# Kernel tuning notes

Hardware: AMD Instinct MI355X
Metric: run time of the kernel (lower is better)

The kernel has to match this reference:

```python
import jax, jax.numpy as jnp
import numpy as np

SAMPLE_RATE = 44100.0
MIN_GAIN, MAX_GAIN = -12.0, 12.0
MIN_Q, MAX_Q = 0.1, 10.0
# (min, max) for the 15 normalized control params, in channel order
PARAM_RANGES = np.array([
    (MIN_GAIN, MAX_GAIN), (20.0, 2000.0), (MIN_Q, MAX_Q),      # low shelf
    (MIN_GAIN, MAX_GAIN), (20.0, 200.0), (MIN_Q, MAX_Q),       # band0 peaking
    (MIN_GAIN, MAX_GAIN), (200.0, 2000.0), (MIN_Q, MAX_Q),     # band1 peaking
    (MIN_GAIN, MAX_GAIN), (2000.0, 12000.0), (MIN_Q, MAX_Q),   # band2 peaking
    (MIN_GAIN, MAX_GAIN), (4000.0, 16000.0), (MIN_Q, MAX_Q),   # high shelf
], dtype=np.float32)


def _biquad(gain_db, f0, q, ftype):
    """RBJ cookbook biquad. Inputs shape (bs,), returns (bs, 6) normalized so a0==1."""
    A = 10.0 ** (gain_db / 40.0)
    w0 = 2.0 * jnp.pi * (f0 / SAMPLE_RATE)
    alpha = jnp.sin(w0) / (2.0 * q)
    cw = jnp.cos(w0)
    sA = jnp.sqrt(A)
    if ftype == 'peaking':
        b0 = 1.0 + alpha * A; b1 = -2.0 * cw; b2 = 1.0 - alpha * A
        a0 = 1.0 + alpha / A; a1 = -2.0 * cw; a2 = 1.0 - alpha / A
    elif ftype == 'low_shelf':
        b0 = A * ((A + 1) - (A - 1) * cw + 2 * sA * alpha)
        b1 = 2 * A * ((A - 1) - (A + 1) * cw)
        b2 = A * ((A + 1) - (A - 1) * cw - 2 * sA * alpha)
        a0 = (A + 1) + (A - 1) * cw + 2 * sA * alpha
        a1 = -2 * ((A - 1) + (A + 1) * cw)
        a2 = (A + 1) + (A - 1) * cw - 2 * sA * alpha
    else:  # high_shelf
        b0 = A * ((A + 1) + (A - 1) * cw + 2 * sA * alpha)
        b1 = -2 * A * ((A - 1) + (A + 1) * cw)
        b2 = A * ((A + 1) + (A - 1) * cw - 2 * sA * alpha)
        a0 = (A + 1) - (A - 1) * cw + 2 * sA * alpha
        a1 = 2 * ((A - 1) - (A + 1) * cw)
        a2 = (A + 1) - (A - 1) * cw - 2 * sA * alpha
    coeffs = jnp.stack([b0, b1, b2, a0, a1, a2], axis=-1)
    return coeffs / a0[..., None]


def _compute_sos(p):
    """p: (bs, 15) denormalized params -> sos (bs, 5, 6)."""
    secs = [
        _biquad(p[:, 0], p[:, 1], p[:, 2], 'low_shelf'),
        _biquad(p[:, 3], p[:, 4], p[:, 5], 'peaking'),
        _biquad(p[:, 6], p[:, 7], p[:, 8], 'peaking'),
        _biquad(p[:, 9], p[:, 10], p[:, 11], 'peaking'),
        _biquad(p[:, 12], p[:, 13], p[:, 14], 'high_shelf'),
    ]
    return jnp.stack(secs, axis=1)


def _sosfilt(sos, x):
    """Cascaded 5-section biquad, direct form II transposed, zero initial state.
    sos: (bs, 5, 6), x: (bs, T) -> (bs, T)."""
    b0, b1, b2 = sos[..., 0], sos[..., 1], sos[..., 2]  # each (bs, 5)
    a1, a2 = sos[..., 4], sos[..., 5]

    def step(carry, xt):
        z1, z2 = carry  # (bs, 5) each
        s = xt  # (bs,)
        z1n, z2n = [], []
        for k in range(5):  # fixed small cascade
            y = b0[:, k] * s + z1[:, k]
            z1n.append(b1[:, k] * s - a1[:, k] * y + z2[:, k])
            z2n.append(b2[:, k] * s - a2[:, k] * y)
            s = y
        return (jnp.stack(z1n, 1), jnp.stack(z2n, 1)), s

    bs = x.shape[0]
    z0 = jnp.zeros((bs, 5), x.dtype)
    _, y = jax.lax.scan(step, (z0, z0), x.T)
    return y.T


def setup_inputs() -> dict:
    key = jax.random.key(0)
    k1, k2 = jax.random.split(key)
    x = jax.random.normal(k1, (32, 1, 131072), dtype=jnp.float32)
    control_params = jax.random.uniform(k2, (32, 15, 1), dtype=jnp.float32)
    return {"x": x, "control_params": control_params}


def reference(x, control_params):
    # denormalize: min + p * (max - min)
    lo = jnp.asarray(PARAM_RANGES[:, 0])
    hi = jnp.asarray(PARAM_RANGES[:, 1])
    p = control_params[:, :, 0]  # (bs, 15)
    p_denorm = lo[None, :] + p * (hi - lo)[None, :]
    sos = _compute_sos(p_denorm)           # (bs, 5, 6)
    y = _sosfilt(sos, x[:, 0, :])          # (bs, T)
    return y[:, None, :], sos
```

## Files before the change

kernel.cpp:

```cpp
#include <hip/hip_runtime.h>
#include <math.h>


#define NB 32
#define LCH 16
#define T_LEN 131072
#define CPB 256
#define BPB 32
#define WPB 128
#define NPOW 13
#define PROW 12
#define PMAT (10 * PROW)

__constant__ double c_lo[15] = {-12.0,   20.0, 0.1,
                                -12.0,   20.0, 0.1,
                                -12.0,  200.0, 0.1,
                                -12.0, 2000.0, 0.1,
                                -12.0, 4000.0, 0.1};
__constant__ double c_hi[15] = { 12.0,  2000.0, 10.0,
                                 12.0,   200.0, 10.0,
                                 12.0,  2000.0, 10.0,
                                 12.0, 12000.0, 10.0,
                                 12.0, 16000.0, 10.0};

__global__ __launch_bounds__(128)
void eq_setup(const float* __restrict__ cp, float* __restrict__ sos_out,
              float* __restrict__ powers)
{
    int b = blockIdx.x;
    int t = threadIdx.x;
    __shared__ float  sc[5][5];
    __shared__ double Abuf[2][10][10];

    if (t < 5) {
        int k = t;
        double p[3];
#pragma unroll
        for (int j = 0; j < 3; ++j) {
            int i = k * 3 + j;
            double pv = (double)cp[b * 15 + i];
            p[j] = c_lo[i] + pv * (c_hi[i] - c_lo[i]);
        }
        double A     = exp(p[0] * (M_LN10 / 40.0));
        double w0    = 2.0 * M_PI * p[1] / 44100.0;
        double alpha = sin(w0) / (2.0 * p[2]);
        double cw    = cos(w0);
        double sA    = sqrt(A);
        double b0, b1, b2, a0, a1, a2;
        if (k == 0) {
            b0 =     A * ((A + 1) - (A - 1) * cw + 2 * sA * alpha);
            b1 = 2 * A * ((A - 1) - (A + 1) * cw);
            b2 =     A * ((A + 1) - (A - 1) * cw - 2 * sA * alpha);
            a0 =          (A + 1) + (A - 1) * cw + 2 * sA * alpha;
            a1 =    -2 * ((A - 1) + (A + 1) * cw);
            a2 =          (A + 1) + (A - 1) * cw - 2 * sA * alpha;
        } else if (k == 4) {
            b0 =     A * ((A + 1) + (A - 1) * cw + 2 * sA * alpha);
            b1 = -2 * A * ((A - 1) + (A + 1) * cw);
            b2 =     A * ((A + 1) + (A - 1) * cw - 2 * sA * alpha);
            a0 =          (A + 1) - (A - 1) * cw + 2 * sA * alpha;
            a1 =     2 * ((A - 1) - (A + 1) * cw);
            a2 =          (A + 1) - (A - 1) * cw - 2 * sA * alpha;
        } else {
            b0 = 1.0 + alpha * A;
            b1 = -2.0 * cw;
            b2 = 1.0 - alpha * A;
            a0 = 1.0 + alpha / A;
            a1 = -2.0 * cw;
            a2 = 1.0 - alpha / A;
        }
        double inv = 1.0 / a0;
        float fb0 = (float)(b0 * inv), fb1 = (float)(b1 * inv), fb2 = (float)(b2 * inv);
        float fa1 = (float)(a1 * inv), fa2 = (float)(a2 * inv);
        float* o = sos_out + (size_t)(b * 5 + k) * 6;
        o[0] = fb0; o[1] = fb1; o[2] = fb2; o[3] = 1.0f; o[4] = fa1; o[5] = fa2;
        sc[k][0] = fb0; sc[k][1] = fb1; sc[k][2] = fb2; sc[k][3] = fa1; sc[k][4] = fa2;
    }
    __syncthreads();

    if (t < 10) {
        double z[10];
#pragma unroll
        for (int i = 0; i < 10; ++i) z[i] = 0.0;
        z[t] = 1.0;
        double s = 0.0;
        double zn[10];
#pragma unroll
        for (int k = 0; k < 5; ++k) {
            double b0 = sc[k][0], b1 = sc[k][1], b2 = sc[k][2];
            double a1 = sc[k][3], a2 = sc[k][4];
            double y = b0 * s + z[2 * k];
            zn[2 * k]     = b1 * s - a1 * y + z[2 * k + 1];
            zn[2 * k + 1] = b2 * s - a2 * y;
            s = y;
        }
#pragma unroll
        for (int r = 0; r < 10; ++r) Abuf[0][r][t] = zn[r];
    }
    __syncthreads();

    int r = t / 10, cc = t % 10;
    int cur = 0;
    for (int sq = 0; sq < 16; ++sq) {
        double acc = 0.0;
        if (t < 100) {
#pragma unroll
            for (int j = 0; j < 10; ++j) acc += Abuf[cur][r][j] * Abuf[cur][j][cc];
        }
        __syncthreads();
        if (t < 100) Abuf[cur ^ 1][r][cc] = acc;
        __syncthreads();
        cur ^= 1;
        if (sq >= 3 && t < 100) {
            int m = sq - 3;
            powers[((size_t)b * NPOW + m) * 100 + t] = (float)Abuf[cur][r][cc];
        }
    }
}

template<bool ACC>
__device__ __forceinline__ void affineT(const float* __restrict__ P,
                                        const float u[10], float v[10])
{
#pragma unroll
    for (int rr = 0; rr < 10; ++rr) {
        const float* rp = P + rr * PROW;
        float a = ACC ? v[rr] : 0.0f;
#pragma unroll
        for (int c = 0; c <= (rr | 1); ++c) a = fmaf(rp[c], u[c], a);
        v[rr] = a;
    }
}

__device__ __forceinline__ void matvecT(const float* __restrict__ P, float v[10])
{
    float u[10];
#pragma unroll
    for (int i = 0; i < 10; ++i) u[i] = v[i];
    affineT<false>(P, u, v);
}

__device__ __forceinline__ void stagePl(float* Pl, const float* __restrict__ powers,
                                        int b, int tid, int nthr)
{
    const float* src = powers + (size_t)b * NPOW * 100;
    for (int i = tid; i < NPOW * PMAT; i += nthr) {
        int c = i % PROW;
        int r = (i / PROW) % 10;
        int m = i / PMAT;
        Pl[i] = (c < 10) ? src[m * 100 + r * 10 + c] : 0.0f;
    }
}

__global__ __launch_bounds__(256)
void eq_pass1(const float* __restrict__ x, const float* __restrict__ sos,
              const float* __restrict__ powers, float* __restrict__ wt)
{
    int blk = blockIdx.x;
    int b = blk >> 5, sp = blk & (BPB - 1);
    int tid = threadIdx.x;
    int w = tid >> 6, lw = tid & 63;

    __shared__ float Pl[NPOW * PMAT];
    stagePl(Pl, powers, b, tid, 256);

    const float* s5 = sos + (size_t)(b * 5) * 6;
    float cb0[5], cb1[5], cb2[5], ca1[5], ca2[5];
#pragma unroll
    for (int k = 0; k < 5; ++k) {
        cb0[k] = s5[k * 6 + 0]; cb1[k] = s5[k * 6 + 1]; cb2[k] = s5[k * 6 + 2];
        ca1[k] = s5[k * 6 + 4]; ca2[k] = s5[k * 6 + 5];
    }

    int c = sp * CPB + tid;
    const float* xp = x + (size_t)b * T_LEN + (size_t)c * LCH;
    float xr[LCH];
#pragma unroll
    for (int t0 = 0; t0 < LCH; t0 += 4) {
        float4 xv = *reinterpret_cast<const float4*>(xp + t0);
        xr[t0] = xv.x; xr[t0 + 1] = xv.y; xr[t0 + 2] = xv.z; xr[t0 + 3] = xv.w;
    }

    float z1[5] = {0, 0, 0, 0, 0}, z2[5] = {0, 0, 0, 0, 0};
#pragma unroll
    for (int j = 0; j < LCH; ++j) {
        float s = xr[j];
#pragma unroll
        for (int k = 0; k < 5; ++k) {
            float yk = fmaf(cb0[k], s, z1[k]);
            float u  = fmaf(cb1[k], s, z2[k]);
            z1[k] = fmaf(-ca1[k], yk, u);
            z2[k] = fmaf(-ca2[k], yk, cb2[k] * s);
            s = yk;
        }
    }
    float sv[10];
#pragma unroll
    for (int k = 0; k < 5; ++k) { sv[2 * k] = z1[k]; sv[2 * k + 1] = z2[k]; }

    __syncthreads();

#pragma unroll
    for (int j = 0; j < 6; ++j) {
        const float* P = Pl + j * PMAT;
        float u[10];
#pragma unroll
        for (int i = 0; i < 10; ++i) u[i] = __shfl_up(sv[i], 1 << j);
        if (lw >= (1 << j)) affineT<true>(P, u, sv);
    }

    if (lw == 63) {
        int wid = sp * 4 + w;
        float* wp = wt + (size_t)(b * WPB + wid) * 10;
#pragma unroll
        for (int i = 0; i < 10; ++i) wp[i] = sv[i];
    }
}

__global__ __launch_bounds__(64)
void eq_scan(const float* __restrict__ powers, const float* __restrict__ wt,
             float* __restrict__ seeds)
{
    int b = blockIdx.x;
    int l = threadIdx.x;

    __shared__ float Pl[NPOW * PMAT];
    stagePl(Pl, powers, b, l, 64);
    __syncthreads();

    const float* wp = wt + (size_t)(b * WPB + 2 * l) * 10;
    float t0[10], t1[10];
#pragma unroll
    for (int i = 0; i < 10; ++i) { t0[i] = wp[i]; t1[i] = wp[10 + i]; }

    float tau[10];
#pragma unroll
    for (int i = 0; i < 10; ++i) tau[i] = t1[i];
    affineT<true>(Pl + 6 * PMAT, t0, tau);

#pragma unroll
    for (int j = 0; j < 6; ++j) {
        const float* P = Pl + (7 + j) * PMAT;
        float u[10];
#pragma unroll
        for (int i = 0; i < 10; ++i) u[i] = __shfl_up(tau[i], 1 << j);
        if (l >= (1 << j)) affineT<true>(P, u, tau);
    }

    float e[10];
#pragma unroll
    for (int i = 0; i < 10; ++i) e[i] = __shfl_up(tau[i], 1);
    if (l == 0) {
#pragma unroll
        for (int i = 0; i < 10; ++i) e[i] = 0.0f;
    }

    float s1[10];
#pragma unroll
    for (int i = 0; i < 10; ++i) s1[i] = t0[i];
    affineT<true>(Pl + 6 * PMAT, e, s1);

    float* sp0 = seeds + (size_t)(b * WPB + 2 * l) * 10;
#pragma unroll
    for (int i = 0; i < 10; ++i) { sp0[i] = e[i]; sp0[10 + i] = s1[i]; }
}

__global__ __launch_bounds__(256)
void eq_pass2(const float* __restrict__ x, const float* __restrict__ sos,
              const float* __restrict__ powers, const float* __restrict__ seeds,
              float* __restrict__ y)
{
    int blk = blockIdx.x;
    int b = blk >> 5, sp = blk & (BPB - 1);
    int tid = threadIdx.x;
    int w = tid >> 6, lw = tid & 63;

    __shared__ float Pl[NPOW * PMAT];
    __shared__ float ys[CPB * 17];
    stagePl(Pl, powers, b, tid, 256);

    const float* s5 = sos + (size_t)(b * 5) * 6;
    float cb0[5], cb1[5], cb2[5], ca1[5], ca2[5];
#pragma unroll
    for (int k = 0; k < 5; ++k) {
        cb0[k] = s5[k * 6 + 0]; cb1[k] = s5[k * 6 + 1]; cb2[k] = s5[k * 6 + 2];
        ca1[k] = s5[k * 6 + 4]; ca2[k] = s5[k * 6 + 5];
    }

    int c = sp * CPB + tid;
    const float* xp = x + (size_t)b * T_LEN + (size_t)c * LCH;
    float xr[LCH];
#pragma unroll
    for (int t0 = 0; t0 < LCH; t0 += 4) {
        float4 xv = *reinterpret_cast<const float4*>(xp + t0);
        xr[t0] = xv.x; xr[t0 + 1] = xv.y; xr[t0 + 2] = xv.z; xr[t0 + 3] = xv.w;
    }

    float z1[5] = {0, 0, 0, 0, 0}, z2[5] = {0, 0, 0, 0, 0};
#pragma unroll
    for (int j = 0; j < LCH; ++j) {
        float s = xr[j];
#pragma unroll
        for (int k = 0; k < 5; ++k) {
            float yk = fmaf(cb0[k], s, z1[k]);
            float u  = fmaf(cb1[k], s, z2[k]);
            z1[k] = fmaf(-ca1[k], yk, u);
            z2[k] = fmaf(-ca2[k], yk, cb2[k] * s);
            s = yk;
        }
    }
    float sv[10];
#pragma unroll
    for (int k = 0; k < 5; ++k) { sv[2 * k] = z1[k]; sv[2 * k + 1] = z2[k]; }

    __syncthreads();

#pragma unroll
    for (int j = 0; j < 6; ++j) {
        const float* P = Pl + j * PMAT;
        float u[10];
#pragma unroll
        for (int i = 0; i < 10; ++i) u[i] = __shfl_up(sv[i], 1 << j);
        if (lw >= (1 << j)) affineT<true>(P, u, sv);
    }
    float es[10];
#pragma unroll
    for (int i = 0; i < 10; ++i) es[i] = __shfl_up(sv[i], 1);
    if (lw == 0) {
#pragma unroll
        for (int i = 0; i < 10; ++i) es[i] = 0.0f;
    }

    int wid = sp * 4 + w;
    const float* sdp = seeds + (size_t)(b * WPB + wid) * 10;
    float F[10];
#pragma unroll
    for (int i = 0; i < 10; ++i) F[i] = sdp[i];
#pragma unroll
    for (int m = 0; m < 6; ++m) {
        if ((lw >> m) & 1) matvecT(Pl + m * PMAT, F);
    }
#pragma unroll
    for (int k = 0; k < 5; ++k) {
        z1[k] = F[2 * k]     + es[2 * k];
        z2[k] = F[2 * k + 1] + es[2 * k + 1];
    }

    float* yl = ys + tid * 17;
#pragma unroll
    for (int j = 0; j < LCH; ++j) {
        float s = xr[j];
#pragma unroll
        for (int k = 0; k < 5; ++k) {
            float yk = fmaf(cb0[k], s, z1[k]);
            float u  = fmaf(cb1[k], s, z2[k]);
            z1[k] = fmaf(-ca1[k], yk, u);
            z2[k] = fmaf(-ca2[k], yk, cb2[k] * s);
            s = yk;
        }
        yl[j] = s;
    }
    __syncthreads();

    float* yg = y + (size_t)b * T_LEN + (size_t)sp * (CPB * LCH);
#pragma unroll
    for (int it = 0; it < (CPB * LCH) / (256 * 4); ++it) {
        int i = (tid + it * 256) * 4;
        int p = (i >> 4) * 17 + (i & 15);
        *reinterpret_cast<float4*>(yg + i) =
            make_float4(ys[p], ys[p + 1], ys[p + 2], ys[p + 3]);
    }
}

extern "C" void kernel_launch(void* const* d_in, const int* in_sizes, int n_in,
                              void* d_out, int out_size, void* d_ws, size_t ws_size,
                              hipStream_t stream)
{
    const float* x  = (const float*)d_in[0];
    const float* cp = (const float*)d_in[1];
    float* out = (float*)d_out;
    float* sos = out + (size_t)NB * T_LEN;

    float* powers = (float*)d_ws;
    float* wt     = powers + (size_t)NB * NPOW * 100;
    float* seeds  = wt + (size_t)NB * WPB * 10;

    eq_setup<<<dim3(NB), dim3(128), 0, stream>>>(cp, sos, powers);
    eq_pass1<<<dim3(NB * BPB), dim3(256), 0, stream>>>(x, sos, powers, wt);
    eq_scan <<<dim3(NB), dim3(64), 0, stream>>>(powers, wt, seeds);
    eq_pass2<<<dim3(NB * BPB), dim3(256), 0, stream>>>(x, sos, powers, seeds, out);
}
```

Baseline: 50.63 us.

## Store per-chunk exclusive scan states in pass1 so pass2 skips recomputation

Pass1 now computes each thread's exclusive in-warp state prefix and writes it to a global workspace, so pass2 no longer reruns the zero-state filter pass and the warp scan; it reads that prefix and filters once. The shared-memory staging of the power matrices is dropped, and matrices are read directly from global memory, which removes a sync and the LDS footprint. Launch bounds now request 4 blocks per CU. This trades recomputation for extra global traffic (10 floats per thread written and read back) and relies on cache hits for the matrix reads.

```diff
diff --git a/kernel.cpp b/kernel.cpp
--- a/kernel.cpp
+++ b/kernel.cpp
@@ -7,10 +7,9 @@
 #define T_LEN 131072
 #define CPB 256
 #define BPB 32
+#define CCH 8192
 #define WPB 128
 #define NPOW 13
-#define PROW 12
-#define PMAT (10 * PROW)
 
 __constant__ double c_lo[15] = {-12.0,   20.0, 0.1,
                                 -12.0,   20.0, 0.1,
@@ -124,7 +123,7 @@
 {
 #pragma unroll
     for (int rr = 0; rr < 10; ++rr) {
-        const float* rp = P + rr * PROW;
+        const float* rp = P + rr * 10;
         float a = ACC ? v[rr] : 0.0f;
 #pragma unroll
         for (int c = 0; c <= (rr | 1); ++c) a = fmaf(rp[c], u[c], a);
@@ -140,29 +139,15 @@
     affineT<false>(P, u, v);
 }
 
-__device__ __forceinline__ void stagePl(float* Pl, const float* __restrict__ powers,
-                                        int b, int tid, int nthr)
-{
-    const float* src = powers + (size_t)b * NPOW * 100;
-    for (int i = tid; i < NPOW * PMAT; i += nthr) {
-        int c = i % PROW;
-        int r = (i / PROW) % 10;
-        int m = i / PMAT;
-        Pl[i] = (c < 10) ? src[m * 100 + r * 10 + c] : 0.0f;
-    }
-}
-
-__global__ __launch_bounds__(256)
+__global__ __launch_bounds__(256, 4)
 void eq_pass1(const float* __restrict__ x, const float* __restrict__ sos,
-              const float* __restrict__ powers, float* __restrict__ wt)
+              const float* __restrict__ powers, float* __restrict__ es_g,
+              float* __restrict__ wt)
 {
     int blk = blockIdx.x;
     int b = blk >> 5, sp = blk & (BPB - 1);
     int tid = threadIdx.x;
     int w = tid >> 6, lw = tid & 63;
-
-    __shared__ float Pl[NPOW * PMAT];
-    stagePl(Pl, powers, b, tid, 256);
 
     const float* s5 = sos + (size_t)(b * 5) * 6;
     float cb0[5], cb1[5], cb2[5], ca1[5], ca2[5];
@@ -198,16 +183,26 @@
 #pragma unroll
     for (int k = 0; k < 5; ++k) { sv[2 * k] = z1[k]; sv[2 * k + 1] = z2[k]; }
 
-    __syncthreads();
-
+    const float* Pb = powers + (size_t)b * NPOW * 100;
 #pragma unroll
     for (int j = 0; j < 6; ++j) {
-        const float* P = Pl + j * PMAT;
+        const float* P = Pb + j * 100;
         float u[10];
 #pragma unroll
         for (int i = 0; i < 10; ++i) u[i] = __shfl_up(sv[i], 1 << j);
         if (lw >= (1 << j)) affineT<true>(P, u, sv);
     }
+
+    float es[10];
+#pragma unroll
+    for (int i = 0; i < 10; ++i) es[i] = __shfl_up(sv[i], 1);
+    if (lw == 0) {
+#pragma unroll
+        for (int i = 0; i < 10; ++i) es[i] = 0.0f;
+    }
+    float* ep = es_g + (size_t)b * 10 * CCH + c;
+#pragma unroll
+    for (int i = 0; i < 10; ++i) ep[(size_t)i * CCH] = es[i];
 
     if (lw == 63) {
         int wid = sp * 4 + w;
@@ -223,10 +218,7 @@
 {
     int b = blockIdx.x;
     int l = threadIdx.x;
-
-    __shared__ float Pl[NPOW * PMAT];
-    stagePl(Pl, powers, b, l, 64);
-    __syncthreads();
+    const float* Pb = powers + (size_t)b * NPOW * 100;
 
     const float* wp = wt + (size_t)(b * WPB + 2 * l) * 10;
     float t0[10], t1[10];
@@ -236,11 +228,11 @@
     float tau[10];
 #pragma unroll
     for (int i = 0; i < 10; ++i) tau[i] = t1[i];
-    affineT<true>(Pl + 6 * PMAT, t0, tau);
+    affineT<true>(Pb + 6 * 100, t0, tau);
 
 #pragma unroll
     for (int j = 0; j < 6; ++j) {
-        const float* P = Pl + (7 + j) * PMAT;
+        const float* P = Pb + (7 + j) * 100;
         float u[10];
 #pragma unroll
         for (int i = 0; i < 10; ++i) u[i] = __shfl_up(tau[i], 1 << j);
@@ -258,26 +250,24 @@
     float s1[10];
 #pragma unroll
     for (int i = 0; i < 10; ++i) s1[i] = t0[i];
-    affineT<true>(Pl + 6 * PMAT, e, s1);
+    affineT<true>(Pb + 6 * 100, e, s1);
 
     float* sp0 = seeds + (size_t)(b * WPB + 2 * l) * 10;
 #pragma unroll
     for (int i = 0; i < 10; ++i) { sp0[i] = e[i]; sp0[10 + i] = s1[i]; }
 }
 
-__global__ __launch_bounds__(256)
+__global__ __launch_bounds__(256, 4)
 void eq_pass2(const float* __restrict__ x, const float* __restrict__ sos,
               const float* __restrict__ powers, const float* __restrict__ seeds,
-              float* __restrict__ y)
+              const float* __restrict__ es_g, float* __restrict__ y)
 {
     int blk = blockIdx.x;
     int b = blk >> 5, sp = blk & (BPB - 1);
     int tid = threadIdx.x;
     int w = tid >> 6, lw = tid & 63;
 
-    __shared__ float Pl[NPOW * PMAT];
     __shared__ float ys[CPB * 17];
-    stagePl(Pl, powers, b, tid, 256);
 
     const float* s5 = sos + (size_t)(b * 5) * 6;
     float cb0[5], cb1[5], cb2[5], ca1[5], ca2[5];
@@ -296,7 +286,26 @@
         xr[t0] = xv.x; xr[t0 + 1] = xv.y; xr[t0 + 2] = xv.z; xr[t0 + 3] = xv.w;
     }
 
-    float z1[5] = {0, 0, 0, 0, 0}, z2[5] = {0, 0, 0, 0, 0};
+    const float* Pb = powers + (size_t)b * NPOW * 100;
+    int wid = sp * 4 + w;
+    const float* sdp = seeds + (size_t)(b * WPB + wid) * 10;
+    float F[10];
+#pragma unroll
+    for (int i = 0; i < 10; ++i) F[i] = sdp[i];
+#pragma unroll
+    for (int m = 0; m < 6; ++m) {
+        if ((lw >> m) & 1) matvecT(Pb + m * 100, F);
+    }
+
+    const float* ep = es_g + (size_t)b * 10 * CCH + c;
+    float z1[5], z2[5];
+#pragma unroll
+    for (int k = 0; k < 5; ++k) {
+        z1[k] = F[2 * k]     + ep[(size_t)(2 * k) * CCH];
+        z2[k] = F[2 * k + 1] + ep[(size_t)(2 * k + 1) * CCH];
+    }
+
+    float* yl = ys + tid * 17;
 #pragma unroll
     for (int j = 0; j < LCH; ++j) {
         float s = xr[j];
@@ -308,56 +317,6 @@
             z2[k] = fmaf(-ca2[k], yk, cb2[k] * s);
             s = yk;
         }
-    }
-    float sv[10];
-#pragma unroll
-    for (int k = 0; k < 5; ++k) { sv[2 * k] = z1[k]; sv[2 * k + 1] = z2[k]; }
-
-    __syncthreads();
-
-#pragma unroll
-    for (int j = 0; j < 6; ++j) {
-        const float* P = Pl + j * PMAT;
-        float u[10];
-#pragma unroll
-        for (int i = 0; i < 10; ++i) u[i] = __shfl_up(sv[i], 1 << j);
-        if (lw >= (1 << j)) affineT<true>(P, u, sv);
-    }
-    float es[10];
-#pragma unroll
-    for (int i = 0; i < 10; ++i) es[i] = __shfl_up(sv[i], 1);
-    if (lw == 0) {
-#pragma unroll
-        for (int i = 0; i < 10; ++i) es[i] = 0.0f;
-    }
-
-    int wid = sp * 4 + w;
-    const float* sdp = seeds + (size_t)(b * WPB + wid) * 10;
-    float F[10];
-#pragma unroll
-    for (int i = 0; i < 10; ++i) F[i] = sdp[i];
-#pragma unroll
-    for (int m = 0; m < 6; ++m) {
-        if ((lw >> m) & 1) matvecT(Pl + m * PMAT, F);
-    }
-#pragma unroll
-    for (int k = 0; k < 5; ++k) {
-        z1[k] = F[2 * k]     + es[2 * k];
-        z2[k] = F[2 * k + 1] + es[2 * k + 1];
-    }
-
-    float* yl = ys + tid * 17;
-#pragma unroll
-    for (int j = 0; j < LCH; ++j) {
-        float s = xr[j];
-#pragma unroll
-        for (int k = 0; k < 5; ++k) {
-            float yk = fmaf(cb0[k], s, z1[k]);
-            float u  = fmaf(cb1[k], s, z2[k]);
-            z1[k] = fmaf(-ca1[k], yk, u);
-            z2[k] = fmaf(-ca2[k], yk, cb2[k] * s);
-            s = yk;
-        }
         yl[j] = s;
     }
     __syncthreads();
@@ -384,9 +343,10 @@
     float* powers = (float*)d_ws;
     float* wt     = powers + (size_t)NB * NPOW * 100;
     float* seeds  = wt + (size_t)NB * WPB * 10;
+    float* es_g   = seeds + (size_t)NB * WPB * 10;
 
     eq_setup<<<dim3(NB), dim3(128), 0, stream>>>(cp, sos, powers);
-    eq_pass1<<<dim3(NB * BPB), dim3(256), 0, stream>>>(x, sos, powers, wt);
+    eq_pass1<<<dim3(NB * BPB), dim3(256), 0, stream>>>(x, sos, powers, es_g, wt);
     eq_scan <<<dim3(NB), dim3(64), 0, stream>>>(powers, wt, seeds);
-    eq_pass2<<<dim3(NB * BPB), dim3(256), 0, stream>>>(x, sos, powers, seeds, out);
-}
+    eq_pass2<<<dim3(NB * BPB), dim3(256), 0, stream>>>(x, sos, powers, seeds, es_g, out);
+}
```

Result: faster. 45.42 us (-10.3%).
